# Kernel tuning notes

Measured on AMD Instinct MI355X. Metric: run time of the kernel, lower is better.

## Reference

```python
import jax, jax.numpy as jnp
import numpy as np

TEMP = 1.0

def setup_inputs() -> dict:
    key = jax.random.key(0)
    k1, k2, k3 = jax.random.split(key, 3)
    B, C, H, W = 8, 256, 64, 64
    h = jax.random.normal(k1, (B, C, H, W), dtype=jnp.float32)
    xs = jax.random.normal(k2, (B, C, H, W), dtype=jnp.float32)
    ys = jax.random.normal(k3, (B, C, H, W), dtype=jnp.float32)
    return {"h": h, "xs": xs, "ys": ys}

def reference(h, xs, ys):
    B, C, H, W = h.shape
    Bs, Cs, Hs, Ws = xs.shape
    hf = h.reshape(B, C, H * W)            # [B, C, N]   N = H*W
    xf = xs.reshape(Bs, Cs, Hs * Ws)       # [B, C, M]   M = Hs*Ws
    yf = ys.reshape(ys.shape[0], ys.shape[1], -1)  # [B, C, M]
    # attention[b, n, m] = sum_c h[b,c,n] * xs[b,c,m]
    attn = jnp.einsum('bcn,bcm->bnm', hf, xf)
    attn = jax.nn.softmax(attn / TEMP, axis=2)  # softmax over support positions m
    # xxs[b, c, n] = sum_m ys[b,c,m] * attn[b,n,m]
    xxs = jnp.einsum('bcm,bnm->bcn', yf, attn)
    return xxs.reshape(B, C, H, W)
```

## Files before the change

kernel.cpp:

```cpp
#include <hip/hip_runtime.h>
#include <stdint.h>

#define B_ 8
#define C_ 256
#define N_ 4096
#define M_ 4096
#define NT 64
#define MT 64
#define PP 72
#define L2E 1.44269504f

typedef _Float16 f16x8 __attribute__((ext_vector_type(8)));
typedef _Float16 f16x4 __attribute__((ext_vector_type(4)));
typedef float f32x4 __attribute__((ext_vector_type(4)));

__device__ __forceinline__ void async16(const _Float16* g, _Float16* l) {
    __builtin_amdgcn_global_load_lds(
        (const __attribute__((address_space(1))) void*)g,
        (__attribute__((address_space(3))) void*)l, 16, 0, 0);
}

__global__ __launch_bounds__(256) void kPre(const float* __restrict__ xs,
                                            const float* __restrict__ ys,
                                            _Float16* __restrict__ kt,
                                            _Float16* __restrict__ vb) {
    int bx = blockIdx.x;
    int t = threadIdx.x;
    if (bx < 2048) {
        __shared__ float tile[64][65];
        int b = bx >> 8, rem = bx & 255;
        int c0 = (rem >> 6) * 64, m0 = (rem & 63) * 64;
        int cl = t >> 4, m4 = (t & 15) * 4;
#pragma unroll
        for (int i = 0; i < 4; i++) {
            int c = c0 + cl + i * 16;
            const float4 v = *(const float4*)(xs + ((size_t)(b * C_ + c) * M_) + m0 + m4);
            tile[m4 + 0][cl + i * 16] = v.x;
            tile[m4 + 1][cl + i * 16] = v.y;
            tile[m4 + 2][cl + i * 16] = v.z;
            tile[m4 + 3][cl + i * 16] = v.w;
        }
        __syncthreads();
        int ml = t >> 4, c4 = (t & 15) * 4;
#pragma unroll
        for (int i = 0; i < 4; i++) {
            int m = m0 + ml + i * 16;
            f16x4 o;
            o[0] = (_Float16)tile[ml + i * 16][c4 + 0];
            o[1] = (_Float16)tile[ml + i * 16][c4 + 1];
            o[2] = (_Float16)tile[ml + i * 16][c4 + 2];
            o[3] = (_Float16)tile[ml + i * 16][c4 + 3];
            *(f16x4*)(kt + ((size_t)(b * M_ + m) * C_) + c0 + c4) = o;
        }
    } else {
        size_t i = ((size_t)(bx - 2048) * 256 + t) * 4;
        float4 v = *(const float4*)(ys + i);
        f16x4 o;
        o[0] = (_Float16)v.x; o[1] = (_Float16)v.y;
        o[2] = (_Float16)v.z; o[3] = (_Float16)v.w;
        *(f16x4*)(vb + i) = o;
    }
}

__global__ __launch_bounds__(256, 2) void kAttn(const float* __restrict__ h,
                                                const _Float16* __restrict__ kt,
                                                const _Float16* __restrict__ vb,
                                                float* __restrict__ out) {
    __shared__ _Float16 sK[2][MT * 256];
    __shared__ _Float16 sP[NT * PP];
    __shared__ float sAlpha[NT];
    __shared__ float sL[NT];
    __shared__ int sFlag[2];

    const int t = threadIdx.x;
    const int w = t >> 6, lane = t & 63, quad = lane >> 4, l15 = lane & 15;
    const int b = blockIdx.x >> 6;
    const int n0 = (blockIdx.x & 63) * NT;
    const int nb = w * 16;
    const int cb = w * 64;

    const _Float16* srcKb = kt + (size_t)b * M_ * C_;
    const _Float16* srcVb = vb + (size_t)b * C_ * M_;

    if (t == 0) { sFlag[0] = 0; sFlag[1] = 0; }

    {
        int cl = t >> 4, n4 = (t & 15) * 4;
        for (int i = 0; i < 16; i++) {
            int c = i * 16 + cl;
            const float4 v = *(const float4*)(h + ((size_t)(b * C_ + c) * N_) + n0 + n4);
            float xv[4] = {v.x, v.y, v.z, v.w};
#pragma unroll
            for (int j = 0; j < 4; j++) {
                int row = n4 + j;
                sK[1][row * 256 + (((c >> 3) ^ (row & 31)) << 3) + (c & 7)] = (_Float16)xv[j];
            }
        }
#pragma unroll
        for (int j = 0; j < 8; j++) {
            int row = w * 16 + j * 2 + (lane >> 5);
            int logi = (lane & 31) ^ (row & 31);
            async16(srcKb + (size_t)row * C_ + logi * 8, &sK[0][(w * 16 + j * 2) * 256]);
        }
    }
    __syncthreads();

    f16x8 qf[8];
    {
        int qrow = nb + l15;
#pragma unroll
        for (int ks = 0; ks < 8; ks++)
            qf[ks] = *(const f16x8*)(&sK[1][qrow * 256 + ((((ks << 2) + quad) ^ (qrow & 31)) << 3)]);
    }

    f32x4 o[4][4];
#pragma unroll
    for (int i = 0; i < 4; i++)
#pragma unroll
        for (int j = 0; j < 4; j++)
            o[i][j] = (f32x4){0.f, 0.f, 0.f, 0.f};

    float mst[4], lp[4];
#pragma unroll
    for (int r = 0; r < 4; r++) { mst[r] = -3.0e38f; lp[r] = 0.f; }

    for (int it = 0; it < M_ / MT; it++) {
        const int cur = it & 1, nxt = cur ^ 1;
        const int m0i = it * MT;
        __syncthreads();

        if (t == 0) sFlag[nxt] = 0;

        if (it + 1 < M_ / MT) {
            const _Float16* srcK = srcKb + (size_t)(m0i + MT) * C_;
#pragma unroll
            for (int j = 0; j < 8; j++) {
                int row = w * 16 + j * 2 + (lane >> 5);
                int logi = (lane & 31) ^ (row & 31);
                async16(srcK + (size_t)row * C_ + logi * 8, &sK[nxt][(w * 16 + j * 2) * 256]);
            }
        }

        f16x8 vf[2][4];
#pragma unroll
        for (int ks = 0; ks < 2; ks++)
#pragma unroll
            for (int ct = 0; ct < 4; ct++) {
                int vrow = cb + ct * 16 + l15;
                vf[ks][ct] = *(const f16x8*)(srcVb + (size_t)vrow * M_ + m0i + ks * 32 + quad * 8);
            }

        f32x4 s[4];
#pragma unroll
        for (int mt = 0; mt < 4; mt++) s[mt] = (f32x4){0.f, 0.f, 0.f, 0.f};
#pragma unroll
        for (int ks = 0; ks < 8; ks++) {
#pragma unroll
            for (int mt = 0; mt < 4; mt++) {
                int krow = mt * 16 + l15;
                f16x8 bk = *(const f16x8*)(&sK[cur][krow * 256 + ((((ks << 2) + quad) ^ (krow & 31)) << 3)]);
                s[mt] = __builtin_amdgcn_mfma_f32_16x16x32_f16(qf[ks], bk, s[mt], 0, 0, 0);
            }
        }

#pragma unroll
        for (int r = 0; r < 4; r++) {
            float rowmax = fmaxf(fmaxf(s[0][r], s[1][r]), fmaxf(s[2][r], s[3][r]));
#pragma unroll
            for (int off = 1; off < 16; off <<= 1)
                rowmax = fmaxf(rowmax, __shfl_xor(rowmax, off, 64));
            float al = 1.0f;
            if (rowmax > mst[r]) {
                al = exp2f((mst[r] - rowmax) * L2E);
                mst[r] = rowmax;
            }
            float psum = 0.f;
#pragma unroll
            for (int mt = 0; mt < 4; mt++) {
                float p = exp2f((s[mt][r] - mst[r]) * L2E);
                s[mt][r] = p;
                psum += p;
            }
            lp[r] = lp[r] * al + psum;
            int row = nb + quad * 4 + r;
            if (l15 == 0) {
                sAlpha[row] = al;
                if (al != 1.0f) atomicOr(&sFlag[cur], 1);
            }
#pragma unroll
            for (int mt = 0; mt < 4; mt++)
                sP[row * PP + mt * 16 + l15] = (_Float16)s[mt][r];
        }
        __syncthreads();

        if (sFlag[cur]) {
            float av[4];
#pragma unroll
            for (int nt = 0; nt < 4; nt++) av[nt] = sAlpha[nt * 16 + l15];
#pragma unroll
            for (int ct = 0; ct < 4; ct++)
#pragma unroll
                for (int nt = 0; nt < 4; nt++) {
                    o[ct][nt][0] *= av[nt];
                    o[ct][nt][1] *= av[nt];
                    o[ct][nt][2] *= av[nt];
                    o[ct][nt][3] *= av[nt];
                }
        }

#pragma unroll
        for (int ks = 0; ks < 2; ks++) {
#pragma unroll
            for (int nt = 0; nt < 4; nt++) {
                f16x8 bp = *(const f16x8*)(sP + (nt * 16 + l15) * PP + ks * 32 + quad * 8);
#pragma unroll
                for (int ct = 0; ct < 4; ct++)
                    o[ct][nt] = __builtin_amdgcn_mfma_f32_16x16x32_f16(vf[ks][ct], bp, o[ct][nt], 0, 0, 0);
            }
        }
    }

#pragma unroll
    for (int r = 0; r < 4; r++) {
#pragma unroll
        for (int off = 1; off < 16; off <<= 1)
            lp[r] += __shfl_xor(lp[r], off, 64);
        if (l15 == 0) sL[nb + quad * 4 + r] = lp[r];
    }
    __syncthreads();
    float linv[4];
#pragma unroll
    for (int nt = 0; nt < 4; nt++) linv[nt] = 1.0f / sL[nt * 16 + l15];
#pragma unroll
    for (int ct = 0; ct < 4; ct++)
#pragma unroll
        for (int nt = 0; nt < 4; nt++)
#pragma unroll
            for (int r = 0; r < 4; r++) {
                int c = cb + ct * 16 + quad * 4 + r;
                out[((size_t)(b * C_ + c)) * N_ + n0 + nt * 16 + l15] = o[ct][nt][r] * linv[nt];
            }
}

extern "C" void kernel_launch(void* const* d_in, const int* in_sizes, int n_in,
                              void* d_out, int out_size, void* d_ws, size_t ws_size,
                              hipStream_t stream) {
    const float* h  = (const float*)d_in[0];
    const float* xs = (const float*)d_in[1];
    const float* ys = (const float*)d_in[2];
    float* out = (float*)d_out;

    _Float16* kt  = (_Float16*)d_ws;
    _Float16* vbb = kt + (size_t)B_ * M_ * C_;

    kPre<<<dim3(2048 + 8192), 256, 0, stream>>>(xs, ys, kt, vbb);
    kAttn<<<dim3(B_ * (N_ / NT)), 256, 0, stream>>>(h, kt, vbb, out);
}
```

Before: 356.7 us.

## Split attention block into 8 waves with M-split QK and cross-wave softmax max

The attention kernel moves from 4 to 8 waves per block. Each pair of waves splits the 64 keys of a tile for QK^T, combining row maxima and partial sums through shared memory, and each wave now owns 32 output channels instead of 64. The K-tile prefetch is reissued after the softmax barrier. The preprocessing kernel gives each block more work: four transposed tiles, or 16 elements of ys per thread. The aim is more waves in flight and fewer registers per wave, at the cost of an extra block-wide barrier on every tile iteration.

```diff
diff --git a/kernel.cpp b/kernel.cpp
--- a/kernel.cpp
+++ b/kernel.cpp
@@ -26,58 +26,70 @@
                                             _Float16* __restrict__ vb) {
     int bx = blockIdx.x;
     int t = threadIdx.x;
-    if (bx < 2048) {
+    if (bx < 512) {
         __shared__ float tile[64][65];
-        int b = bx >> 8, rem = bx & 255;
-        int c0 = (rem >> 6) * 64, m0 = (rem & 63) * 64;
-        int cl = t >> 4, m4 = (t & 15) * 4;
-#pragma unroll
-        for (int i = 0; i < 4; i++) {
-            int c = c0 + cl + i * 16;
-            const float4 v = *(const float4*)(xs + ((size_t)(b * C_ + c) * M_) + m0 + m4);
-            tile[m4 + 0][cl + i * 16] = v.x;
-            tile[m4 + 1][cl + i * 16] = v.y;
-            tile[m4 + 2][cl + i * 16] = v.z;
-            tile[m4 + 3][cl + i * 16] = v.w;
-        }
-        __syncthreads();
-        int ml = t >> 4, c4 = (t & 15) * 4;
-#pragma unroll
-        for (int i = 0; i < 4; i++) {
-            int m = m0 + ml + i * 16;
-            f16x4 o;
-            o[0] = (_Float16)tile[ml + i * 16][c4 + 0];
-            o[1] = (_Float16)tile[ml + i * 16][c4 + 1];
-            o[2] = (_Float16)tile[ml + i * 16][c4 + 2];
-            o[3] = (_Float16)tile[ml + i * 16][c4 + 3];
-            *(f16x4*)(kt + ((size_t)(b * M_ + m) * C_) + c0 + c4) = o;
+        int b = bx >> 6, c0 = ((bx >> 4) & 3) * 64, ms = (bx & 15) * 256;
+#pragma unroll
+        for (int mi = 0; mi < 4; mi++) {
+            int m0 = ms + mi * 64;
+            if (mi) __syncthreads();
+            int cl = t >> 4, m4 = (t & 15) * 4;
+#pragma unroll
+            for (int i = 0; i < 4; i++) {
+                int c = c0 + cl + i * 16;
+                const float4 v = *(const float4*)(xs + ((size_t)(b * C_ + c) * M_) + m0 + m4);
+                tile[m4 + 0][cl + i * 16] = v.x;
+                tile[m4 + 1][cl + i * 16] = v.y;
+                tile[m4 + 2][cl + i * 16] = v.z;
+                tile[m4 + 3][cl + i * 16] = v.w;
+            }
+            __syncthreads();
+            int ml = t >> 4, c4 = (t & 15) * 4;
+#pragma unroll
+            for (int i = 0; i < 4; i++) {
+                int m = m0 + ml + i * 16;
+                f16x4 o;
+                o[0] = (_Float16)tile[ml + i * 16][c4 + 0];
+                o[1] = (_Float16)tile[ml + i * 16][c4 + 1];
+                o[2] = (_Float16)tile[ml + i * 16][c4 + 2];
+                o[3] = (_Float16)tile[ml + i * 16][c4 + 3];
+                *(f16x4*)(kt + ((size_t)(b * M_ + m) * C_) + c0 + c4) = o;
+            }
         }
     } else {
-        size_t i = ((size_t)(bx - 2048) * 256 + t) * 4;
-        float4 v = *(const float4*)(ys + i);
-        f16x4 o;
-        o[0] = (_Float16)v.x; o[1] = (_Float16)v.y;
-        o[2] = (_Float16)v.z; o[3] = (_Float16)v.w;
-        *(f16x4*)(vb + i) = o;
-    }
-}
-
-__global__ __launch_bounds__(256, 2) void kAttn(const float* __restrict__ h,
+        size_t base = ((size_t)(bx - 512) * 256 + t) * 16;
+#pragma unroll
+        for (int j = 0; j < 2; j++) {
+            float4 a = *(const float4*)(ys + base + j * 8);
+            float4 c = *(const float4*)(ys + base + j * 8 + 4);
+            f16x8 o;
+            o[0] = (_Float16)a.x; o[1] = (_Float16)a.y;
+            o[2] = (_Float16)a.z; o[3] = (_Float16)a.w;
+            o[4] = (_Float16)c.x; o[5] = (_Float16)c.y;
+            o[6] = (_Float16)c.z; o[7] = (_Float16)c.w;
+            *(f16x8*)(vb + base + j * 8) = o;
+        }
+    }
+}
+
+__global__ __launch_bounds__(512, 4) void kAttn(const float* __restrict__ h,
                                                 const _Float16* __restrict__ kt,
                                                 const _Float16* __restrict__ vb,
                                                 float* __restrict__ out) {
     __shared__ _Float16 sK[2][MT * 256];
     __shared__ _Float16 sP[NT * PP];
+    __shared__ float sMaxP[2][NT];
+    __shared__ float sLP[2][NT];
     __shared__ float sAlpha[NT];
-    __shared__ float sL[NT];
     __shared__ int sFlag[2];
 
     const int t = threadIdx.x;
     const int w = t >> 6, lane = t & 63, quad = lane >> 4, l15 = lane & 15;
+    const int wn = w & 3, wm = w >> 2;
     const int b = blockIdx.x >> 6;
     const int n0 = (blockIdx.x & 63) * NT;
-    const int nb = w * 16;
-    const int cb = w * 64;
+    const int nb = wn * 16;
+    const int cb = w * 32;
 
     const _Float16* srcKb = kt + (size_t)b * M_ * C_;
     const _Float16* srcVb = vb + (size_t)b * C_ * M_;
@@ -86,8 +98,9 @@
 
     {
         int cl = t >> 4, n4 = (t & 15) * 4;
-        for (int i = 0; i < 16; i++) {
-            int c = i * 16 + cl;
+#pragma unroll
+        for (int i = 0; i < 8; i++) {
+            int c = i * 32 + cl;
             const float4 v = *(const float4*)(h + ((size_t)(b * C_ + c) * N_) + n0 + n4);
             float xv[4] = {v.x, v.y, v.z, v.w};
 #pragma unroll
@@ -96,12 +109,6 @@
                 sK[1][row * 256 + (((c >> 3) ^ (row & 31)) << 3) + (c & 7)] = (_Float16)xv[j];
             }
         }
-#pragma unroll
-        for (int j = 0; j < 8; j++) {
-            int row = w * 16 + j * 2 + (lane >> 5);
-            int logi = (lane & 31) ^ (row & 31);
-            async16(srcKb + (size_t)row * C_ + logi * 8, &sK[0][(w * 16 + j * 2) * 256]);
-        }
     }
     __syncthreads();
 
@@ -112,10 +119,18 @@
         for (int ks = 0; ks < 8; ks++)
             qf[ks] = *(const f16x8*)(&sK[1][qrow * 256 + ((((ks << 2) + quad) ^ (qrow & 31)) << 3)]);
     }
-
-    f32x4 o[4][4];
-#pragma unroll
-    for (int i = 0; i < 4; i++)
+    __syncthreads();
+
+#pragma unroll
+    for (int j = 0; j < 4; j++) {
+        int row = w * 8 + j * 2 + (lane >> 5);
+        int logi = (lane & 31) ^ (row & 31);
+        async16(srcKb + (size_t)row * C_ + logi * 8, &sK[0][(w * 8 + j * 2) * 256]);
+    }
+
+    f32x4 o[2][4];
+#pragma unroll
+    for (int i = 0; i < 2; i++)
 #pragma unroll
         for (int j = 0; j < 4; j++)
             o[i][j] = (f32x4){0.f, 0.f, 0.f, 0.f};
@@ -125,50 +140,47 @@
     for (int r = 0; r < 4; r++) { mst[r] = -3.0e38f; lp[r] = 0.f; }
 
     for (int it = 0; it < M_ / MT; it++) {
-        const int cur = it & 1, nxt = cur ^ 1;
+        const int cur = it & 1;
         const int m0i = it * MT;
         __syncthreads();
-
-        if (t == 0) sFlag[nxt] = 0;
-
-        if (it + 1 < M_ / MT) {
-            const _Float16* srcK = srcKb + (size_t)(m0i + MT) * C_;
-#pragma unroll
-            for (int j = 0; j < 8; j++) {
-                int row = w * 16 + j * 2 + (lane >> 5);
-                int logi = (lane & 31) ^ (row & 31);
-                async16(srcK + (size_t)row * C_ + logi * 8, &sK[nxt][(w * 16 + j * 2) * 256]);
-            }
-        }
-
-        f16x8 vf[2][4];
+        if (t == 0) sFlag[cur ^ 1] = 0;
+
+        f16x8 vf[2][2];
 #pragma unroll
         for (int ks = 0; ks < 2; ks++)
 #pragma unroll
-            for (int ct = 0; ct < 4; ct++) {
+            for (int ct = 0; ct < 2; ct++) {
                 int vrow = cb + ct * 16 + l15;
                 vf[ks][ct] = *(const f16x8*)(srcVb + (size_t)vrow * M_ + m0i + ks * 32 + quad * 8);
             }
 
-        f32x4 s[4];
-#pragma unroll
-        for (int mt = 0; mt < 4; mt++) s[mt] = (f32x4){0.f, 0.f, 0.f, 0.f};
+        f32x4 s[2];
+        s[0] = (f32x4){0.f, 0.f, 0.f, 0.f};
+        s[1] = (f32x4){0.f, 0.f, 0.f, 0.f};
 #pragma unroll
         for (int ks = 0; ks < 8; ks++) {
 #pragma unroll
-            for (int mt = 0; mt < 4; mt++) {
-                int krow = mt * 16 + l15;
+            for (int l = 0; l < 2; l++) {
+                int krow = wm * 32 + l * 16 + l15;
                 f16x8 bk = *(const f16x8*)(&sK[cur][krow * 256 + ((((ks << 2) + quad) ^ (krow & 31)) << 3)]);
-                s[mt] = __builtin_amdgcn_mfma_f32_16x16x32_f16(qf[ks], bk, s[mt], 0, 0, 0);
+                s[l] = __builtin_amdgcn_mfma_f32_16x16x32_f16(qf[ks], bk, s[l], 0, 0, 0);
             }
         }
 
 #pragma unroll
         for (int r = 0; r < 4; r++) {
-            float rowmax = fmaxf(fmaxf(s[0][r], s[1][r]), fmaxf(s[2][r], s[3][r]));
+            float pm = fmaxf(s[0][r], s[1][r]);
 #pragma unroll
             for (int off = 1; off < 16; off <<= 1)
-                rowmax = fmaxf(rowmax, __shfl_xor(rowmax, off, 64));
+                pm = fmaxf(pm, __shfl_xor(pm, off, 64));
+            if (l15 == 0) sMaxP[wm][nb + quad * 4 + r] = pm;
+        }
+        __syncthreads();
+
+#pragma unroll
+        for (int r = 0; r < 4; r++) {
+            int row = nb + quad * 4 + r;
+            float rowmax = fmaxf(sMaxP[0][row], sMaxP[1][row]);
             float al = 1.0f;
             if (rowmax > mst[r]) {
                 al = exp2f((mst[r] - rowmax) * L2E);
@@ -176,29 +188,38 @@
             }
             float psum = 0.f;
 #pragma unroll
-            for (int mt = 0; mt < 4; mt++) {
-                float p = exp2f((s[mt][r] - mst[r]) * L2E);
-                s[mt][r] = p;
+            for (int l = 0; l < 2; l++) {
+                float p = exp2f((s[l][r] - mst[r]) * L2E);
+                s[l][r] = p;
                 psum += p;
             }
             lp[r] = lp[r] * al + psum;
-            int row = nb + quad * 4 + r;
             if (l15 == 0) {
                 sAlpha[row] = al;
                 if (al != 1.0f) atomicOr(&sFlag[cur], 1);
             }
 #pragma unroll
-            for (int mt = 0; mt < 4; mt++)
-                sP[row * PP + mt * 16 + l15] = (_Float16)s[mt][r];
+            for (int l = 0; l < 2; l++)
+                sP[row * PP + wm * 32 + l * 16 + l15] = (_Float16)s[l][r];
         }
         __syncthreads();
+
+        if (it + 1 < M_ / MT) {
+            const _Float16* srcK = srcKb + (size_t)(m0i + MT) * C_;
+#pragma unroll
+            for (int j = 0; j < 4; j++) {
+                int row = w * 8 + j * 2 + (lane >> 5);
+                int logi = (lane & 31) ^ (row & 31);
+                async16(srcK + (size_t)row * C_ + logi * 8, &sK[cur ^ 1][(w * 8 + j * 2) * 256]);
+            }
+        }
 
         if (sFlag[cur]) {
             float av[4];
 #pragma unroll
             for (int nt = 0; nt < 4; nt++) av[nt] = sAlpha[nt * 16 + l15];
 #pragma unroll
-            for (int ct = 0; ct < 4; ct++)
+            for (int ct = 0; ct < 2; ct++)
 #pragma unroll
                 for (int nt = 0; nt < 4; nt++) {
                     o[ct][nt][0] *= av[nt];
@@ -214,7 +235,7 @@
             for (int nt = 0; nt < 4; nt++) {
                 f16x8 bp = *(const f16x8*)(sP + (nt * 16 + l15) * PP + ks * 32 + quad * 8);
 #pragma unroll
-                for (int ct = 0; ct < 4; ct++)
+                for (int ct = 0; ct < 2; ct++)
                     o[ct][nt] = __builtin_amdgcn_mfma_f32_16x16x32_f16(vf[ks][ct], bp, o[ct][nt], 0, 0, 0);
             }
         }
@@ -225,14 +246,17 @@
 #pragma unroll
         for (int off = 1; off < 16; off <<= 1)
             lp[r] += __shfl_xor(lp[r], off, 64);
-        if (l15 == 0) sL[nb + quad * 4 + r] = lp[r];
+        if (l15 == 0) sLP[wm][nb + quad * 4 + r] = lp[r];
     }
     __syncthreads();
     float linv[4];
 #pragma unroll
-    for (int nt = 0; nt < 4; nt++) linv[nt] = 1.0f / sL[nt * 16 + l15];
-#pragma unroll
-    for (int ct = 0; ct < 4; ct++)
+    for (int nt = 0; nt < 4; nt++) {
+        int n = nt * 16 + l15;
+        linv[nt] = 1.0f / (sLP[0][n] + sLP[1][n]);
+    }
+#pragma unroll
+    for (int ct = 0; ct < 2; ct++)
 #pragma unroll
         for (int nt = 0; nt < 4; nt++)
 #pragma unroll
@@ -253,6 +277,6 @@
     _Float16* kt  = (_Float16*)d_ws;
     _Float16* vbb = kt + (size_t)B_ * M_ * C_;
 
-    kPre<<<dim3(2048 + 8192), 256, 0, stream>>>(xs, ys, kt, vbb);
-    kAttn<<<dim3(B_ * (N_ / NT)), 256, 0, stream>>>(h, kt, vbb, out);
-}
+    kPre<<<dim3(512 + 2048), 256, 0, stream>>>(xs, ys, kt, vbb);
+    kAttn<<<dim3(B_ * (N_ / NT)), 512, 0, stream>>>(h, kt, vbb, out);
+}
```

New measurement: 719.3 us. +101.6%, slower.
